# Kernel tuning notes

Measured on AMD Instinct MI355X. Metric: run time of the kernel, lower is better.

The kernel has to match this reference:

```python
import jax, jax.numpy as jnp
import numpy as np

DIM = 1024
NUM_HEADS = 16
HEAD_DIM = DIM // NUM_HEADS
SCALE = HEAD_DIM ** -0.5


def setup_inputs() -> dict:
    key = jax.random.key(0)
    k1, k2, k3, k4 = jax.random.split(key, 4)
    x = jax.random.normal(k1, (4, 2048, DIM), dtype=jnp.float32)
    # nn.Linear weights: out = x @ W.T + b ; store as [out, in] like torch
    w_qkv = jax.random.normal(k2, (3 * DIM, DIM), dtype=jnp.float32) * (DIM ** -0.5)
    w_proj = jax.random.normal(k3, (DIM, DIM), dtype=jnp.float32) * (DIM ** -0.5)
    b_proj = jax.random.normal(k4, (DIM,), dtype=jnp.float32) * 0.01
    return {"x": x, "w_qkv": w_qkv, "w_proj": w_proj, "b_proj": b_proj}


def reference(x, w_qkv, w_proj, b_proj):
    B, N, C = x.shape
    H, D = NUM_HEADS, HEAD_DIM
    qkv = jnp.einsum('bnc,oc->bno', x, w_qkv)            # [B,N,3C]
    qkv = qkv.reshape(B, N, 3, H, D).transpose(2, 0, 3, 1, 4)  # [3,B,H,N,D]
    q, k, v = qkv[0] * SCALE, qkv[1], qkv[2]
    attn = jax.nn.softmax(jnp.einsum('bhnd,bhmd->bhnm', q, k), axis=-1)
    out = jnp.einsum('bhnm,bhmd->bhnd', attn, v)          # [B,H,N,D]
    out = out.transpose(0, 2, 1, 3).reshape(B, N, C)
    return jnp.einsum('bnc,oc->bno', out, w_proj) + b_proj
```

## Files before the change

### kernel.cpp

```cpp
#include <hip/hip_runtime.h>
#include <cstdint>

#define DIM   1024
#define NH    16
#define HD    64
#define SEQ   2048
#define BATCH 4
#define QK_EXP2_SCALE 0.18033688011112042f

typedef _Float16 half8  __attribute__((ext_vector_type(8)));
typedef __fp16   fp16x2 __attribute__((ext_vector_type(2)));
typedef float    f32x4  __attribute__((ext_vector_type(4)));

#define GLOBAL_AS __attribute__((address_space(1)))
#define LDS_AS    __attribute__((address_space(3)))

__device__ __forceinline__ ushort f2h(float f) {
  union { _Float16 h; ushort u; } c; c.h = (_Float16)f; return c.u;
}
__device__ __forceinline__ void async_cp16(const ushort* g, ushort* l) {
  __builtin_amdgcn_global_load_lds((const GLOBAL_AS uint32_t*)g,
                                   (LDS_AS uint32_t*)l, 16, 0, 0);
}

__global__ __launch_bounds__(256) void cvt3_f32_to_f16(
    const float4* __restrict__ x, const float4* __restrict__ wq,
    const float4* __restrict__ wp, ushort4* __restrict__ xo,
    ushort4* __restrict__ wqo, ushort4* __restrict__ wpo) {
  int i = blockIdx.x * 256 + threadIdx.x;
  const float4* src; ushort4* dst; int j;
  if (i < 2097152)      { src = x;  dst = xo;  j = i; }
  else if (i < 2883584) { src = wq; dst = wqo; j = i - 2097152; }
  else                  { src = wp; dst = wpo; j = i - 2883584; }
  float4 v = src[j];
  dst[j] = make_ushort4(f2h(v.x), f2h(v.y), f2h(v.z), f2h(v.w));
}

__global__ __launch_bounds__(256, 2) void gemm_bt256(
    const ushort* __restrict__ A, const ushort* __restrict__ Bt,
    ushort* __restrict__ Ch, int M, int N, int K) {
  __shared__ ushort As[128 * 64];
  __shared__ ushort Bs[256 * 64];
  const int t    = threadIdx.x;
  const int w    = t >> 6;
  const int lane = t & 63;
  const int quad = lane >> 4;
  const int l16  = lane & 15;
  const int wm   = w >> 1, wn = w & 1;

  const int num_n = N >> 8;
  const int SUPER = 8;
  const int bid   = blockIdx.x;
  const int strip = bid / (SUPER * num_n);
  const int rem   = bid % (SUPER * num_n);
  const int m0 = (strip * SUPER + (rem % SUPER)) * 128;
  const int n0 = (rem / SUPER) * 256;

  f32x4 acc[4][8];
  #pragma unroll
  for (int it = 0; it < 4; ++it)
    #pragma unroll
    for (int jt = 0; jt < 8; ++jt) acc[it][jt] = (f32x4){0, 0, 0, 0};

  const int srow = lane >> 3;
  const int scol = ((lane & 7) ^ (lane >> 3)) * 8;
  const int cxa  = l16 & 7;

  for (int k0 = 0; k0 < K; k0 += 64) {
    __syncthreads();
    #pragma unroll
    for (int p = 0; p < 4; ++p) {
      const int rbase = w * 32 + p * 8;
      async_cp16(&A[(size_t)(m0 + rbase + srow) * K + k0 + scol], &As[rbase * 64]);
    }
    #pragma unroll
    for (int p = 0; p < 8; ++p) {
      const int rbase = w * 64 + p * 8;
      async_cp16(&Bt[(size_t)(n0 + rbase + srow) * K + k0 + scol], &Bs[rbase * 64]);
    }
    __syncthreads();
    #pragma unroll
    for (int kk = 0; kk < 2; ++kk) {
      const int ko = ((kk * 4 + quad) ^ cxa) * 8;
      half8 a[4];
      #pragma unroll
      for (int it = 0; it < 4; ++it)
        a[it] = *(const half8*)&As[(wm * 64 + it * 16 + l16) * 64 + ko];
      #pragma unroll
      for (int jt = 0; jt < 8; ++jt) {
        half8 b = *(const half8*)&Bs[(wn * 128 + jt * 16 + l16) * 64 + ko];
        #pragma unroll
        for (int it = 0; it < 4; ++it)
          acc[it][jt] = __builtin_amdgcn_mfma_f32_16x16x32_f16(a[it], b, acc[it][jt], 0, 0, 0);
      }
    }
  }

  #pragma unroll
  for (int it = 0; it < 4; ++it)
    #pragma unroll
    for (int jt = 0; jt < 8; ++jt) {
      const int colbase = n0 + wn * 128 + jt * 16;
      const float qs = (colbase < DIM) ? QK_EXP2_SCALE : 1.0f;
      #pragma unroll
      for (int i = 0; i < 4; ++i) {
        int row = m0 + wm * 64 + it * 16 + quad * 4 + i;
        int col = n0 + wn * 128 + jt * 16 + l16;
        Ch[(size_t)row * N + col] = f2h(acc[it][jt][i] * qs);
      }
    }
}

__global__ __launch_bounds__(256) void gemm_bt128(
    const ushort* __restrict__ A, const ushort* __restrict__ Bt,
    float* __restrict__ Cf, const float* __restrict__ bias,
    int M, int N, int K) {
  __shared__ ushort As[128 * 64];
  __shared__ ushort Bs[128 * 64];
  const int t    = threadIdx.x;
  const int w    = t >> 6;
  const int lane = t & 63;
  const int quad = lane >> 4;
  const int l16  = lane & 15;
  const int wm   = w >> 1, wn = w & 1;

  const int num_n = N >> 7;
  const int SUPER = 8;
  const int bid   = blockIdx.x;
  const int strip = bid / (SUPER * num_n);
  const int rem   = bid % (SUPER * num_n);
  const int m0 = (strip * SUPER + (rem % SUPER)) * 128;
  const int n0 = (rem / SUPER) * 128;

  f32x4 acc[4][4];
  #pragma unroll
  for (int it = 0; it < 4; ++it)
    #pragma unroll
    for (int jt = 0; jt < 4; ++jt) acc[it][jt] = (f32x4){0, 0, 0, 0};

  const int srow = lane >> 3;
  const int scol = ((lane & 7) ^ (lane >> 3)) * 8;
  const int cxa  = l16 & 7;

  for (int k0 = 0; k0 < K; k0 += 64) {
    __syncthreads();
    #pragma unroll
    for (int p = 0; p < 4; ++p) {
      const int rbase = w * 32 + p * 8;
      async_cp16(&A[(size_t)(m0 + rbase + srow) * K + k0 + scol], &As[rbase * 64]);
      async_cp16(&Bt[(size_t)(n0 + rbase + srow) * K + k0 + scol], &Bs[rbase * 64]);
    }
    __syncthreads();
    #pragma unroll
    for (int kk = 0; kk < 2; ++kk) {
      const int ko = ((kk * 4 + quad) ^ cxa) * 8;
      half8 a[4], b[4];
      #pragma unroll
      for (int it = 0; it < 4; ++it)
        a[it] = *(const half8*)&As[(wm * 64 + it * 16 + l16) * 64 + ko];
      #pragma unroll
      for (int jt = 0; jt < 4; ++jt)
        b[jt] = *(const half8*)&Bs[(wn * 64 + jt * 16 + l16) * 64 + ko];
      #pragma unroll
      for (int it = 0; it < 4; ++it)
        #pragma unroll
        for (int jt = 0; jt < 4; ++jt)
          acc[it][jt] = __builtin_amdgcn_mfma_f32_16x16x32_f16(a[it], b[jt], acc[it][jt], 0, 0, 0);
    }
  }

  #pragma unroll
  for (int it = 0; it < 4; ++it)
    #pragma unroll
    for (int jt = 0; jt < 4; ++jt)
      #pragma unroll
      for (int i = 0; i < 4; ++i) {
        int row = m0 + wm * 64 + it * 16 + quad * 4 + i;
        int col = n0 + wn * 64 + jt * 16 + l16;
        Cf[(size_t)row * N + col] = acc[it][jt][i] + bias[col];
      }
}

__global__ __launch_bounds__(256, 2) void attn_mfma(
    const ushort* __restrict__ qkv, ushort* __restrict__ attn_out) {
  constexpr int LDT = 68;
  constexpr int NT  = SEQ / 64;
  __shared__ ushort Qs[256 * LDT];
  __shared__ ushort Ks[2][64 * LDT];
  __shared__ ushort Vt[2][64 * LDT];

  const int t    = threadIdx.x;
  const int w    = t >> 6;
  const int lane = t & 63;
  const int quad = lane >> 4;
  const int l16  = lane & 15;
  const int q0 = blockIdx.x * 256;
  const int h  = blockIdx.y;
  const int b  = blockIdx.z;

  const int srow = t >> 2;
  const int sseg = t & 3;
  const int vp   = t & 31;
  const int vs   = t >> 5;
  const int vpos = ((vp >> 4) << 5) + (((vp >> 1) & 3) << 3)
                 + (((vp >> 3) & 1) << 2) + ((vp & 1) << 1);

  #pragma unroll
  for (int pass = 0; pass < 2; ++pass) {
    const int qrow = pass * 128 + (t >> 1), qseg = t & 1;
    const ushort* qp = qkv + (size_t)(b * SEQ + q0 + qrow) * (3 * DIM)
                       + h * HD + qseg * 32;
    #pragma unroll
    for (int e = 0; e < 4; ++e)
      *(int4*)&Qs[qrow * LDT + qseg * 32 + e * 8] = *(const int4*)(qp + e * 8);
  }

  f32x4 ot[4][4];
  float lacc[4] = {0.0f, 0.0f, 0.0f, 0.0f};
  #pragma unroll
  for (int qt = 0; qt < 4; ++qt)
    #pragma unroll
    for (int nt = 0; nt < 4; ++nt) ot[qt][nt] = (f32x4){0, 0, 0, 0};

  const ushort* kbase = qkv + (size_t)(b * SEQ + srow) * (3 * DIM)
                        + DIM + h * HD + sseg * 16;
  const ushort* vbase = qkv + (size_t)(b * SEQ + 2 * vp) * (3 * DIM)
                        + 2 * DIM + h * HD + vs * 8;
  const size_t tstep = (size_t)64 * (3 * DIM);

  int4 kr0 = *(const int4*)(kbase + 0);
  int4 kr1 = *(const int4*)(kbase + 8);
  int4 vr0 = *(const int4*)(vbase);
  int4 vr1 = *(const int4*)(vbase + 3 * DIM);
  {
    *(int4*)&Ks[0][srow * LDT + sseg * 16 + 0] = kr0;
    *(int4*)&Ks[0][srow * LDT + sseg * 16 + 8] = kr1;
    union { int4 v; ushort u[8]; } r0, r1;
    r0.v = vr0; r1.v = vr1;
    #pragma unroll
    for (int j = 0; j < 8; ++j) {
      uint pk = (uint)r0.u[j] | ((uint)r1.u[j] << 16);
      *(uint*)&Vt[0][(vs * 8 + j) * LDT + vpos] = pk;
    }
  }

  for (int c = 0; c < NT; ++c) {
    const int buf = c & 1;
    __syncthreads();

    const int cn = (c + 1 < NT) ? (c + 1) : 0;
    {
      const ushort* kp = kbase + (size_t)cn * tstep;
      const ushort* vv = vbase + (size_t)cn * tstep;
      kr0 = *(const int4*)(kp + 0);
      kr1 = *(const int4*)(kp + 8);
      vr0 = *(const int4*)(vv);
      vr1 = *(const int4*)(vv + 3 * DIM);
    }
    __builtin_amdgcn_sched_barrier(0);

    f32x4 st[4][4];
    #pragma unroll
    for (int qt = 0; qt < 4; ++qt)
      #pragma unroll
      for (int kt = 0; kt < 4; ++kt) st[qt][kt] = (f32x4){0, 0, 0, 0};
    __builtin_amdgcn_s_setprio(1);
    #pragma unroll
    for (int kk = 0; kk < 2; ++kk) {
      half8 kfr[4], qfr[4];
      #pragma unroll
      for (int kt = 0; kt < 4; ++kt)
        kfr[kt] = *(const half8*)&Ks[buf][(kt * 16 + l16) * LDT + kk * 32 + quad * 8];
      #pragma unroll
      for (int qt = 0; qt < 4; ++qt)
        qfr[qt] = *(const half8*)&Qs[(w * 64 + qt * 16 + l16) * LDT + kk * 32 + quad * 8];
      #pragma unroll
      for (int qt = 0; qt < 4; ++qt)
        #pragma unroll
        for (int kt = 0; kt < 4; ++kt)
          st[qt][kt] = __builtin_amdgcn_mfma_f32_16x16x32_f16(kfr[kt], qfr[qt], st[qt][kt], 0, 0, 0);
    }
    __builtin_amdgcn_s_setprio(0);

    union { half8 h; uint u[4]; } pf[4][2];
    #pragma unroll
    for (int qt = 0; qt < 4; ++qt) {
      float p[4][4];
      #pragma unroll
      for (int kt = 0; kt < 4; ++kt)
        #pragma unroll
        for (int i = 0; i < 4; ++i) {
          p[kt][i] = __builtin_amdgcn_exp2f(st[qt][kt][i]);
          lacc[qt] += p[kt][i];
        }
      #pragma unroll
      for (int kc = 0; kc < 2; ++kc) {
        union { fp16x2 h; uint u; } c01, c23, c45, c67;
        c01.h = __builtin_amdgcn_cvt_pkrtz(p[2 * kc][0], p[2 * kc][1]);
        c23.h = __builtin_amdgcn_cvt_pkrtz(p[2 * kc][2], p[2 * kc][3]);
        c45.h = __builtin_amdgcn_cvt_pkrtz(p[2 * kc + 1][0], p[2 * kc + 1][1]);
        c67.h = __builtin_amdgcn_cvt_pkrtz(p[2 * kc + 1][2], p[2 * kc + 1][3]);
        pf[qt][kc].u[0] = c01.u; pf[qt][kc].u[1] = c23.u;
        pf[qt][kc].u[2] = c45.u; pf[qt][kc].u[3] = c67.u;
      }
    }

    __builtin_amdgcn_s_setprio(1);
    #pragma unroll
    for (int kc = 0; kc < 2; ++kc) {
      half8 vfr[4];
      #pragma unroll
      for (int nt = 0; nt < 4; ++nt)
        vfr[nt] = *(const half8*)&Vt[buf][(nt * 16 + l16) * LDT + kc * 32 + quad * 8];
      #pragma unroll
      for (int qt = 0; qt < 4; ++qt)
        #pragma unroll
        for (int nt = 0; nt < 4; ++nt)
          ot[qt][nt] = __builtin_amdgcn_mfma_f32_16x16x32_f16(vfr[nt], pf[qt][kc].h, ot[qt][nt], 0, 0, 0);
    }
    __builtin_amdgcn_s_setprio(0);

    {
      const int nb = buf ^ 1;
      *(int4*)&Ks[nb][srow * LDT + sseg * 16 + 0] = kr0;
      *(int4*)&Ks[nb][srow * LDT + sseg * 16 + 8] = kr1;
      union { int4 v; ushort u[8]; } r0, r1;
      r0.v = vr0; r1.v = vr1;
      #pragma unroll
      for (int j = 0; j < 8; ++j) {
        uint pk = (uint)r0.u[j] | ((uint)r1.u[j] << 16);
        *(uint*)&Vt[nb][(vs * 8 + j) * LDT + vpos] = pk;
      }
    }
  }

  __syncthreads();
  #pragma unroll
  for (int qt = 0; qt < 4; ++qt) {
    float lsum = lacc[qt];
    lsum += __shfl_xor(lsum, 16);
    lsum += __shfl_xor(lsum, 32);
    float inv = 1.0f / lsum;
    #pragma unroll
    for (int nt = 0; nt < 4; ++nt)
      #pragma unroll
      for (int i = 0; i < 4; ++i)
        Qs[(w * 64 + qt * 16 + l16) * LDT + nt * 16 + quad * 4 + i] =
            f2h(ot[qt][nt][i] * inv);
  }
  __syncthreads();
  #pragma unroll
  for (int pass = 0; pass < 2; ++pass) {
    const int orow = pass * 128 + (t >> 1), oseg = t & 1;
    size_t gbase = (size_t)(b * SEQ + q0 + orow) * DIM + h * HD + oseg * 32;
    #pragma unroll
    for (int e = 0; e < 4; ++e)
      *(int4*)&attn_out[gbase + e * 8] = *(const int4*)&Qs[orow * LDT + oseg * 32 + e * 8];
  }
}

extern "C" void kernel_launch(void* const* d_in, const int* in_sizes, int n_in,
                              void* d_out, int out_size, void* d_ws, size_t ws_size,
                              hipStream_t stream) {
  const float* x      = (const float*)d_in[0];
  const float* w_qkv  = (const float*)d_in[1];
  const float* w_proj = (const float*)d_in[2];
  const float* b_proj = (const float*)d_in[3];

  char* ws = (char*)d_ws;
  ushort* x_h   = (ushort*)(ws + 0);
  ushort* wq_h  = (ushort*)(ws + 16777216);
  ushort* wp_h  = (ushort*)(ws + 23068672);
  ushort* qkv_h = (ushort*)(ws + 25165824);
  ushort* at_h  = (ushort*)(ws + 75497472);

  cvt3_f32_to_f16<<<12288, 256, 0, stream>>>(
      (const float4*)x, (const float4*)w_qkv, (const float4*)w_proj,
      (ushort4*)x_h, (ushort4*)wq_h, (ushort4*)wp_h);

  gemm_bt256<<<64 * 12, 256, 0, stream>>>(x_h, wq_h, qkv_h, 8192, 3072, 1024);
  attn_mfma<<<dim3(8, 16, 4), 256, 0, stream>>>(qkv_h, at_h);
  gemm_bt128<<<64 * 8, 256, 0, stream>>>(at_h, wp_h, (float*)d_out,
                                         b_proj, 8192, 1024, 1024);
}
```

Before: 262.9 us.

## Restructure attention to 8 waves with register-resident Q and split K/V loaders

The attention kernel goes from 4 to 8 waves per block of 256 queries, each wave handling 32 queries. Q fragments stay in registers instead of LDS, and the LDS shrinks to a shared K/V double buffer. Half the threads load and transpose V while the other half load K, and the global loads now sit after the compute phase rather than being prefetched into registers. The block index is flattened so consecutive blocks cover different heads and batches. The aim is higher occupancy and fewer LDS reads, at the risk of exposing global-load latency because the register prefetch is gone.

```diff
diff --git a/kernel.cpp b/kernel.cpp
--- a/kernel.cpp
+++ b/kernel.cpp
@@ -181,46 +181,32 @@
       }
 }
 
-__global__ __launch_bounds__(256, 2) void attn_mfma(
+__global__ __launch_bounds__(512, 4) void attn_mfma(
     const ushort* __restrict__ qkv, ushort* __restrict__ attn_out) {
   constexpr int LDT = 68;
   constexpr int NT  = SEQ / 64;
-  __shared__ ushort Qs[256 * LDT];
-  __shared__ ushort Ks[2][64 * LDT];
-  __shared__ ushort Vt[2][64 * LDT];
+  __shared__ ushort KV[4 * 64 * LDT];
 
   const int t    = threadIdx.x;
   const int w    = t >> 6;
   const int lane = t & 63;
   const int quad = lane >> 4;
   const int l16  = lane & 15;
-  const int q0 = blockIdx.x * 256;
-  const int h  = blockIdx.y;
-  const int b  = blockIdx.z;
-
-  const int srow = t >> 2;
-  const int sseg = t & 3;
+
+  const int id = blockIdx.x;
+  const int hb = id & 63;
+  const int q0 = (id >> 6) * 256;
+  const int h  = hb & 15;
+  const int b  = hb >> 4;
+
+  const bool vrole = (t < 256);
   const int vp   = t & 31;
-  const int vs   = t >> 5;
+  const int vs   = (t >> 5) & 7;
   const int vpos = ((vp >> 4) << 5) + (((vp >> 1) & 3) << 3)
                  + (((vp >> 3) & 1) << 2) + ((vp & 1) << 1);
-
-  #pragma unroll
-  for (int pass = 0; pass < 2; ++pass) {
-    const int qrow = pass * 128 + (t >> 1), qseg = t & 1;
-    const ushort* qp = qkv + (size_t)(b * SEQ + q0 + qrow) * (3 * DIM)
-                       + h * HD + qseg * 32;
-    #pragma unroll
-    for (int e = 0; e < 4; ++e)
-      *(int4*)&Qs[qrow * LDT + qseg * 32 + e * 8] = *(const int4*)(qp + e * 8);
-  }
-
-  f32x4 ot[4][4];
-  float lacc[4] = {0.0f, 0.0f, 0.0f, 0.0f};
-  #pragma unroll
-  for (int qt = 0; qt < 4; ++qt)
-    #pragma unroll
-    for (int nt = 0; nt < 4; ++nt) ot[qt][nt] = (f32x4){0, 0, 0, 0};
+  const int u    = t & 255;
+  const int srow = u >> 2;
+  const int sseg = u & 3;
 
   const ushort* kbase = qkv + (size_t)(b * SEQ + srow) * (3 * DIM)
                         + DIM + h * HD + sseg * 16;
@@ -228,63 +214,69 @@
                         + 2 * DIM + h * HD + vs * 8;
   const size_t tstep = (size_t)64 * (3 * DIM);
 
-  int4 kr0 = *(const int4*)(kbase + 0);
-  int4 kr1 = *(const int4*)(kbase + 8);
-  int4 vr0 = *(const int4*)(vbase);
-  int4 vr1 = *(const int4*)(vbase + 3 * DIM);
+  half8 qreg[2][2];
+  #pragma unroll
+  for (int qt = 0; qt < 2; ++qt)
+    #pragma unroll
+    for (int kk = 0; kk < 2; ++kk)
+      qreg[qt][kk] = *(const half8*)(qkv
+          + (size_t)(b * SEQ + q0 + w * 32 + qt * 16 + l16) * (3 * DIM)
+          + h * HD + kk * 32 + quad * 8);
+
   {
-    *(int4*)&Ks[0][srow * LDT + sseg * 16 + 0] = kr0;
-    *(int4*)&Ks[0][srow * LDT + sseg * 16 + 8] = kr1;
-    union { int4 v; ushort u[8]; } r0, r1;
-    r0.v = vr0; r1.v = vr1;
-    #pragma unroll
-    for (int j = 0; j < 8; ++j) {
-      uint pk = (uint)r0.u[j] | ((uint)r1.u[j] << 16);
-      *(uint*)&Vt[0][(vs * 8 + j) * LDT + vpos] = pk;
-    }
-  }
+    if (vrole) {
+      union { int4 v; ushort u[8]; } r0, r1;
+      r0.v = *(const int4*)(vbase);
+      r1.v = *(const int4*)(vbase + 3 * DIM);
+      ushort* Vd = &KV[2 * 64 * LDT];
+      #pragma unroll
+      for (int j = 0; j < 8; ++j) {
+        uint pk = (uint)r0.u[j] | ((uint)r1.u[j] << 16);
+        *(uint*)&Vd[(vs * 8 + j) * LDT + vpos] = pk;
+      }
+    } else {
+      ushort* Kd = &KV[0];
+      *(int4*)&Kd[srow * LDT + sseg * 16 + 0] = *(const int4*)(kbase + 0);
+      *(int4*)&Kd[srow * LDT + sseg * 16 + 8] = *(const int4*)(kbase + 8);
+    }
+  }
+
+  f32x4 ot[2][4];
+  float lacc[2] = {0.0f, 0.0f};
+  #pragma unroll
+  for (int qt = 0; qt < 2; ++qt)
+    #pragma unroll
+    for (int nt = 0; nt < 4; ++nt) ot[qt][nt] = (f32x4){0, 0, 0, 0};
 
   for (int c = 0; c < NT; ++c) {
     const int buf = c & 1;
-    __syncthreads();
-
-    const int cn = (c + 1 < NT) ? (c + 1) : 0;
-    {
-      const ushort* kp = kbase + (size_t)cn * tstep;
-      const ushort* vv = vbase + (size_t)cn * tstep;
-      kr0 = *(const int4*)(kp + 0);
-      kr1 = *(const int4*)(kp + 8);
-      vr0 = *(const int4*)(vv);
-      vr1 = *(const int4*)(vv + 3 * DIM);
-    }
-    __builtin_amdgcn_sched_barrier(0);
-
-    f32x4 st[4][4];
-    #pragma unroll
-    for (int qt = 0; qt < 4; ++qt)
+    const ushort* Kb = &KV[buf * 64 * LDT];
+    const ushort* Vb = &KV[(2 + buf) * 64 * LDT];
+    __syncthreads();
+
+    f32x4 st[2][4];
+    #pragma unroll
+    for (int qt = 0; qt < 2; ++qt)
       #pragma unroll
       for (int kt = 0; kt < 4; ++kt) st[qt][kt] = (f32x4){0, 0, 0, 0};
     __builtin_amdgcn_s_setprio(1);
     #pragma unroll
     for (int kk = 0; kk < 2; ++kk) {
-      half8 kfr[4], qfr[4];
+      half8 kfr[4];
       #pragma unroll
       for (int kt = 0; kt < 4; ++kt)
-        kfr[kt] = *(const half8*)&Ks[buf][(kt * 16 + l16) * LDT + kk * 32 + quad * 8];
-      #pragma unroll
-      for (int qt = 0; qt < 4; ++qt)
-        qfr[qt] = *(const half8*)&Qs[(w * 64 + qt * 16 + l16) * LDT + kk * 32 + quad * 8];
-      #pragma unroll
-      for (int qt = 0; qt < 4; ++qt)
+        kfr[kt] = *(const half8*)&Kb[(kt * 16 + l16) * LDT + kk * 32 + quad * 8];
+      #pragma unroll
+      for (int qt = 0; qt < 2; ++qt)
         #pragma unroll
         for (int kt = 0; kt < 4; ++kt)
-          st[qt][kt] = __builtin_amdgcn_mfma_f32_16x16x32_f16(kfr[kt], qfr[qt], st[qt][kt], 0, 0, 0);
+          st[qt][kt] = __builtin_amdgcn_mfma_f32_16x16x32_f16(kfr[kt], qreg[qt][kk], st[qt][kt], 0, 0, 0);
     }
     __builtin_amdgcn_s_setprio(0);
 
-    union { half8 h; uint u[4]; } pf[4][2];
-    #pragma unroll
-    for (int qt = 0; qt < 4; ++qt) {
+    union { half8 h; uint u[4]; } pf[2][2];
+    #pragma unroll
+    for (int qt = 0; qt < 2; ++qt) {
       float p[4][4];
       #pragma unroll
       for (int kt = 0; kt < 4; ++kt)
@@ -311,32 +303,40 @@
       half8 vfr[4];
       #pragma unroll
       for (int nt = 0; nt < 4; ++nt)
-        vfr[nt] = *(const half8*)&Vt[buf][(nt * 16 + l16) * LDT + kc * 32 + quad * 8];
-      #pragma unroll
-      for (int qt = 0; qt < 4; ++qt)
+        vfr[nt] = *(const half8*)&Vb[(nt * 16 + l16) * LDT + kc * 32 + quad * 8];
+      #pragma unroll
+      for (int qt = 0; qt < 2; ++qt)
         #pragma unroll
         for (int nt = 0; nt < 4; ++nt)
           ot[qt][nt] = __builtin_amdgcn_mfma_f32_16x16x32_f16(vfr[nt], pf[qt][kc].h, ot[qt][nt], 0, 0, 0);
     }
     __builtin_amdgcn_s_setprio(0);
 
-    {
+    if (c + 1 < NT) {
       const int nb = buf ^ 1;
-      *(int4*)&Ks[nb][srow * LDT + sseg * 16 + 0] = kr0;
-      *(int4*)&Ks[nb][srow * LDT + sseg * 16 + 8] = kr1;
-      union { int4 v; ushort u[8]; } r0, r1;
-      r0.v = vr0; r1.v = vr1;
-      #pragma unroll
-      for (int j = 0; j < 8; ++j) {
-        uint pk = (uint)r0.u[j] | ((uint)r1.u[j] << 16);
-        *(uint*)&Vt[nb][(vs * 8 + j) * LDT + vpos] = pk;
+      if (vrole) {
+        const ushort* vv = vbase + (size_t)(c + 1) * tstep;
+        union { int4 v; ushort u[8]; } r0, r1;
+        r0.v = *(const int4*)(vv);
+        r1.v = *(const int4*)(vv + 3 * DIM);
+        ushort* Vd = &KV[(2 + nb) * 64 * LDT];
+        #pragma unroll
+        for (int j = 0; j < 8; ++j) {
+          uint pk = (uint)r0.u[j] | ((uint)r1.u[j] << 16);
+          *(uint*)&Vd[(vs * 8 + j) * LDT + vpos] = pk;
+        }
+      } else {
+        const ushort* kp = kbase + (size_t)(c + 1) * tstep;
+        ushort* Kd = &KV[nb * 64 * LDT];
+        *(int4*)&Kd[srow * LDT + sseg * 16 + 0] = *(const int4*)(kp + 0);
+        *(int4*)&Kd[srow * LDT + sseg * 16 + 8] = *(const int4*)(kp + 8);
       }
     }
   }
 
   __syncthreads();
   #pragma unroll
-  for (int qt = 0; qt < 4; ++qt) {
+  for (int qt = 0; qt < 2; ++qt) {
     float lsum = lacc[qt];
     lsum += __shfl_xor(lsum, 16);
     lsum += __shfl_xor(lsum, 32);
@@ -345,17 +345,16 @@
     for (int nt = 0; nt < 4; ++nt)
       #pragma unroll
       for (int i = 0; i < 4; ++i)
-        Qs[(w * 64 + qt * 16 + l16) * LDT + nt * 16 + quad * 4 + i] =
+        KV[(w * 32 + qt * 16 + l16) * LDT + nt * 16 + quad * 4 + i] =
             f2h(ot[qt][nt][i] * inv);
   }
   __syncthreads();
-  #pragma unroll
-  for (int pass = 0; pass < 2; ++pass) {
-    const int orow = pass * 128 + (t >> 1), oseg = t & 1;
+  {
+    const int orow = t >> 1, oseg = t & 1;
     size_t gbase = (size_t)(b * SEQ + q0 + orow) * DIM + h * HD + oseg * 32;
     #pragma unroll
     for (int e = 0; e < 4; ++e)
-      *(int4*)&attn_out[gbase + e * 8] = *(const int4*)&Qs[orow * LDT + oseg * 32 + e * 8];
+      *(int4*)&attn_out[gbase + e * 8] = *(const int4*)&KV[orow * LDT + oseg * 32 + e * 8];
   }
 }
 
@@ -379,7 +378,7 @@
       (ushort4*)x_h, (ushort4*)wq_h, (ushort4*)wp_h);
 
   gemm_bt256<<<64 * 12, 256, 0, stream>>>(x_h, wq_h, qkv_h, 8192, 3072, 1024);
-  attn_mfma<<<dim3(8, 16, 4), 256, 0, stream>>>(qkv_h, at_h);
+  attn_mfma<<<512, 512, 0, stream>>>(qkv_h, at_h);
   gemm_bt128<<<64 * 8, 256, 0, stream>>>(at_h, wp_h, (float*)d_out,
                                          b_proj, 8192, 1024, 1024);
 }
```

New measurement: 426.4 us. 1.62x slower.

## Keep Q in registers and stream 128-key tiles in attention

Applied to the files above, without the earlier changes.

The attention kernel now loads the Q fragments straight into registers rather than staging them in LDS, and processes K/V in 128-key chunks, so half as many barriers are needed. The next tile's global loads are no longer prefetched into registers before compute; they are issued after compute and written directly to LDS. Blocks are linearised so consecutive blocks cover different heads and batches of the same query range, and the occupancy hint of 2 blocks is dropped. The aim is to cut LDS traffic and sync overhead, but it raises register pressure and may expose global load latency that was previously hidden.

```diff
diff --git a/kernel.cpp b/kernel.cpp
--- a/kernel.cpp
+++ b/kernel.cpp
@@ -181,22 +181,24 @@
       }
 }
 
-__global__ __launch_bounds__(256, 2) void attn_mfma(
+__global__ __launch_bounds__(256) void attn_mfma(
     const ushort* __restrict__ qkv, ushort* __restrict__ attn_out) {
-  constexpr int LDT = 68;
-  constexpr int NT  = SEQ / 64;
-  __shared__ ushort Qs[256 * LDT];
-  __shared__ ushort Ks[2][64 * LDT];
-  __shared__ ushort Vt[2][64 * LDT];
+  constexpr int LDK = 68;
+  constexpr int LDV = 132;
+  constexpr int NT  = SEQ / 128;
+  __shared__ ushort SH[2 * 128 * LDK + 2 * 64 * LDV];
 
   const int t    = threadIdx.x;
   const int w    = t >> 6;
   const int lane = t & 63;
   const int quad = lane >> 4;
   const int l16  = lane & 15;
-  const int q0 = blockIdx.x * 256;
-  const int h  = blockIdx.y;
-  const int b  = blockIdx.z;
+
+  const int id = blockIdx.x;
+  const int hb = id & 63;
+  const int q0 = (id >> 6) * 256;
+  const int h  = hb & 15;
+  const int b  = hb >> 4;
 
   const int srow = t >> 2;
   const int sseg = t & 3;
@@ -205,131 +207,140 @@
   const int vpos = ((vp >> 4) << 5) + (((vp >> 1) & 3) << 3)
                  + (((vp >> 3) & 1) << 2) + ((vp & 1) << 1);
 
-  #pragma unroll
-  for (int pass = 0; pass < 2; ++pass) {
-    const int qrow = pass * 128 + (t >> 1), qseg = t & 1;
-    const ushort* qp = qkv + (size_t)(b * SEQ + q0 + qrow) * (3 * DIM)
-                       + h * HD + qseg * 32;
-    #pragma unroll
-    for (int e = 0; e < 4; ++e)
-      *(int4*)&Qs[qrow * LDT + qseg * 32 + e * 8] = *(const int4*)(qp + e * 8);
-  }
-
-  f32x4 ot[4][4];
-  float lacc[4] = {0.0f, 0.0f, 0.0f, 0.0f};
-  #pragma unroll
-  for (int qt = 0; qt < 4; ++qt)
-    #pragma unroll
-    for (int nt = 0; nt < 4; ++nt) ot[qt][nt] = (f32x4){0, 0, 0, 0};
-
   const ushort* kbase = qkv + (size_t)(b * SEQ + srow) * (3 * DIM)
                         + DIM + h * HD + sseg * 16;
   const ushort* vbase = qkv + (size_t)(b * SEQ + 2 * vp) * (3 * DIM)
                         + 2 * DIM + h * HD + vs * 8;
-  const size_t tstep = (size_t)64 * (3 * DIM);
-
-  int4 kr0 = *(const int4*)(kbase + 0);
-  int4 kr1 = *(const int4*)(kbase + 8);
-  int4 vr0 = *(const int4*)(vbase);
-  int4 vr1 = *(const int4*)(vbase + 3 * DIM);
+  const size_t rstep = (size_t)64 * (3 * DIM);
+  const size_t tstep = (size_t)128 * (3 * DIM);
+
+  half8 qreg[4][2];
+  #pragma unroll
+  for (int qt = 0; qt < 4; ++qt)
+    #pragma unroll
+    for (int kk = 0; kk < 2; ++kk)
+      qreg[qt][kk] = *(const half8*)(qkv
+          + (size_t)(b * SEQ + q0 + w * 64 + qt * 16 + l16) * (3 * DIM)
+          + h * HD + kk * 32 + quad * 8);
+
   {
-    *(int4*)&Ks[0][srow * LDT + sseg * 16 + 0] = kr0;
-    *(int4*)&Ks[0][srow * LDT + sseg * 16 + 8] = kr1;
-    union { int4 v; ushort u[8]; } r0, r1;
-    r0.v = vr0; r1.v = vr1;
-    #pragma unroll
-    for (int j = 0; j < 8; ++j) {
-      uint pk = (uint)r0.u[j] | ((uint)r1.u[j] << 16);
-      *(uint*)&Vt[0][(vs * 8 + j) * LDT + vpos] = pk;
-    }
-  }
+    ushort* Kd = &SH[0];
+    ushort* Vd = &SH[2 * 128 * LDK];
+    #pragma unroll
+    for (int r = 0; r < 2; ++r) {
+      const ushort* kp = kbase + (size_t)r * rstep;
+      *(int4*)&Kd[(srow + r * 64) * LDK + sseg * 16 + 0] = *(const int4*)(kp + 0);
+      *(int4*)&Kd[(srow + r * 64) * LDK + sseg * 16 + 8] = *(const int4*)(kp + 8);
+      const ushort* vv = vbase + (size_t)r * rstep;
+      union { int4 v; ushort u[8]; } r0, r1;
+      r0.v = *(const int4*)(vv);
+      r1.v = *(const int4*)(vv + 3 * DIM);
+      #pragma unroll
+      for (int j = 0; j < 8; ++j) {
+        uint pk = (uint)r0.u[j] | ((uint)r1.u[j] << 16);
+        *(uint*)&Vd[(vs * 8 + j) * LDV + r * 64 + vpos] = pk;
+      }
+    }
+  }
+
+  f32x4 ot[4][4];
+  float lacc[4] = {0.0f, 0.0f, 0.0f, 0.0f};
+  #pragma unroll
+  for (int qt = 0; qt < 4; ++qt)
+    #pragma unroll
+    for (int nt = 0; nt < 4; ++nt) ot[qt][nt] = (f32x4){0, 0, 0, 0};
 
   for (int c = 0; c < NT; ++c) {
     const int buf = c & 1;
-    __syncthreads();
-
-    const int cn = (c + 1 < NT) ? (c + 1) : 0;
-    {
-      const ushort* kp = kbase + (size_t)cn * tstep;
-      const ushort* vv = vbase + (size_t)cn * tstep;
-      kr0 = *(const int4*)(kp + 0);
-      kr1 = *(const int4*)(kp + 8);
-      vr0 = *(const int4*)(vv);
-      vr1 = *(const int4*)(vv + 3 * DIM);
-    }
-    __builtin_amdgcn_sched_barrier(0);
-
-    f32x4 st[4][4];
-    #pragma unroll
-    for (int qt = 0; qt < 4; ++qt)
-      #pragma unroll
-      for (int kt = 0; kt < 4; ++kt) st[qt][kt] = (f32x4){0, 0, 0, 0};
-    __builtin_amdgcn_s_setprio(1);
-    #pragma unroll
-    for (int kk = 0; kk < 2; ++kk) {
-      half8 kfr[4], qfr[4];
-      #pragma unroll
-      for (int kt = 0; kt < 4; ++kt)
-        kfr[kt] = *(const half8*)&Ks[buf][(kt * 16 + l16) * LDT + kk * 32 + quad * 8];
+    const ushort* Kb = &SH[buf * 128 * LDK];
+    const ushort* Vb = &SH[2 * 128 * LDK + buf * 64 * LDV];
+    __syncthreads();
+
+    #pragma unroll
+    for (int half = 0; half < 2; ++half) {
+      f32x4 st[4][4];
       #pragma unroll
       for (int qt = 0; qt < 4; ++qt)
-        qfr[qt] = *(const half8*)&Qs[(w * 64 + qt * 16 + l16) * LDT + kk * 32 + quad * 8];
-      #pragma unroll
-      for (int qt = 0; qt < 4; ++qt)
+        #pragma unroll
+        for (int kt = 0; kt < 4; ++kt) st[qt][kt] = (f32x4){0, 0, 0, 0};
+      __builtin_amdgcn_s_setprio(1);
+      #pragma unroll
+      for (int kk = 0; kk < 2; ++kk) {
+        half8 kfr[4];
         #pragma unroll
         for (int kt = 0; kt < 4; ++kt)
-          st[qt][kt] = __builtin_amdgcn_mfma_f32_16x16x32_f16(kfr[kt], qfr[qt], st[qt][kt], 0, 0, 0);
-    }
-    __builtin_amdgcn_s_setprio(0);
-
-    union { half8 h; uint u[4]; } pf[4][2];
-    #pragma unroll
-    for (int qt = 0; qt < 4; ++qt) {
-      float p[4][4];
-      #pragma unroll
-      for (int kt = 0; kt < 4; ++kt)
-        #pragma unroll
-        for (int i = 0; i < 4; ++i) {
-          p[kt][i] = __builtin_amdgcn_exp2f(st[qt][kt][i]);
-          lacc[qt] += p[kt][i];
+          kfr[kt] = *(const half8*)&Kb[(half * 64 + kt * 16 + l16) * LDK
+                                       + kk * 32 + quad * 8];
+        #pragma unroll
+        for (int qt = 0; qt < 4; ++qt)
+          #pragma unroll
+          for (int kt = 0; kt < 4; ++kt)
+            st[qt][kt] = __builtin_amdgcn_mfma_f32_16x16x32_f16(
+                kfr[kt], qreg[qt][kk], st[qt][kt], 0, 0, 0);
+      }
+      __builtin_amdgcn_s_setprio(0);
+
+      union { half8 h; uint u[4]; } pf[4][2];
+      #pragma unroll
+      for (int qt = 0; qt < 4; ++qt) {
+        float p[4][4];
+        #pragma unroll
+        for (int kt = 0; kt < 4; ++kt)
+          #pragma unroll
+          for (int i = 0; i < 4; ++i) {
+            p[kt][i] = __builtin_amdgcn_exp2f(st[qt][kt][i]);
+            lacc[qt] += p[kt][i];
+          }
+        #pragma unroll
+        for (int kc = 0; kc < 2; ++kc) {
+          union { fp16x2 h; uint u; } c01, c23, c45, c67;
+          c01.h = __builtin_amdgcn_cvt_pkrtz(p[2 * kc][0], p[2 * kc][1]);
+          c23.h = __builtin_amdgcn_cvt_pkrtz(p[2 * kc][2], p[2 * kc][3]);
+          c45.h = __builtin_amdgcn_cvt_pkrtz(p[2 * kc + 1][0], p[2 * kc + 1][1]);
+          c67.h = __builtin_amdgcn_cvt_pkrtz(p[2 * kc + 1][2], p[2 * kc + 1][3]);
+          pf[qt][kc].u[0] = c01.u; pf[qt][kc].u[1] = c23.u;
+          pf[qt][kc].u[2] = c45.u; pf[qt][kc].u[3] = c67.u;
         }
+      }
+
+      __builtin_amdgcn_s_setprio(1);
       #pragma unroll
       for (int kc = 0; kc < 2; ++kc) {
-        union { fp16x2 h; uint u; } c01, c23, c45, c67;
-        c01.h = __builtin_amdgcn_cvt_pkrtz(p[2 * kc][0], p[2 * kc][1]);
-        c23.h = __builtin_amdgcn_cvt_pkrtz(p[2 * kc][2], p[2 * kc][3]);
-        c45.h = __builtin_amdgcn_cvt_pkrtz(p[2 * kc + 1][0], p[2 * kc + 1][1]);
-        c67.h = __builtin_amdgcn_cvt_pkrtz(p[2 * kc + 1][2], p[2 * kc + 1][3]);
-        pf[qt][kc].u[0] = c01.u; pf[qt][kc].u[1] = c23.u;
-        pf[qt][kc].u[2] = c45.u; pf[qt][kc].u[3] = c67.u;
-      }
-    }
-
-    __builtin_amdgcn_s_setprio(1);
-    #pragma unroll
-    for (int kc = 0; kc < 2; ++kc) {
-      half8 vfr[4];
-      #pragma unroll
-      for (int nt = 0; nt < 4; ++nt)
-        vfr[nt] = *(const half8*)&Vt[buf][(nt * 16 + l16) * LDT + kc * 32 + quad * 8];
-      #pragma unroll
-      for (int qt = 0; qt < 4; ++qt)
+        half8 vfr[4];
         #pragma unroll
         for (int nt = 0; nt < 4; ++nt)
-          ot[qt][nt] = __builtin_amdgcn_mfma_f32_16x16x32_f16(vfr[nt], pf[qt][kc].h, ot[qt][nt], 0, 0, 0);
-    }
-    __builtin_amdgcn_s_setprio(0);
-
-    {
+          vfr[nt] = *(const half8*)&Vb[(nt * 16 + l16) * LDV
+                                       + half * 64 + kc * 32 + quad * 8];
+        #pragma unroll
+        for (int qt = 0; qt < 4; ++qt)
+          #pragma unroll
+          for (int nt = 0; nt < 4; ++nt)
+            ot[qt][nt] = __builtin_amdgcn_mfma_f32_16x16x32_f16(
+                vfr[nt], pf[qt][kc].h, ot[qt][nt], 0, 0, 0);
+      }
+      __builtin_amdgcn_s_setprio(0);
+    }
+
+    if (c + 1 < NT) {
       const int nb = buf ^ 1;
-      *(int4*)&Ks[nb][srow * LDT + sseg * 16 + 0] = kr0;
-      *(int4*)&Ks[nb][srow * LDT + sseg * 16 + 8] = kr1;
-      union { int4 v; ushort u[8]; } r0, r1;
-      r0.v = vr0; r1.v = vr1;
-      #pragma unroll
-      for (int j = 0; j < 8; ++j) {
-        uint pk = (uint)r0.u[j] | ((uint)r1.u[j] << 16);
-        *(uint*)&Vt[nb][(vs * 8 + j) * LDT + vpos] = pk;
+      ushort* Kd = &SH[nb * 128 * LDK];
+      ushort* Vd = &SH[2 * 128 * LDK + nb * 64 * LDV];
+      const ushort* kp0 = kbase + (size_t)(c + 1) * tstep;
+      const ushort* vv0 = vbase + (size_t)(c + 1) * tstep;
+      #pragma unroll
+      for (int r = 0; r < 2; ++r) {
+        const ushort* kp = kp0 + (size_t)r * rstep;
+        *(int4*)&Kd[(srow + r * 64) * LDK + sseg * 16 + 0] = *(const int4*)(kp + 0);
+        *(int4*)&Kd[(srow + r * 64) * LDK + sseg * 16 + 8] = *(const int4*)(kp + 8);
+        const ushort* vv = vv0 + (size_t)r * rstep;
+        union { int4 v; ushort u[8]; } r0, r1;
+        r0.v = *(const int4*)(vv);
+        r1.v = *(const int4*)(vv + 3 * DIM);
+        #pragma unroll
+        for (int j = 0; j < 8; ++j) {
+          uint pk = (uint)r0.u[j] | ((uint)r1.u[j] << 16);
+          *(uint*)&Vd[(vs * 8 + j) * LDV + r * 64 + vpos] = pk;
+        }
       }
     }
   }
@@ -345,7 +356,7 @@
     for (int nt = 0; nt < 4; ++nt)
       #pragma unroll
       for (int i = 0; i < 4; ++i)
-        Qs[(w * 64 + qt * 16 + l16) * LDT + nt * 16 + quad * 4 + i] =
+        SH[(w * 64 + qt * 16 + l16) * LDK + nt * 16 + quad * 4 + i] =
             f2h(ot[qt][nt][i] * inv);
   }
   __syncthreads();
@@ -355,7 +366,7 @@
     size_t gbase = (size_t)(b * SEQ + q0 + orow) * DIM + h * HD + oseg * 32;
     #pragma unroll
     for (int e = 0; e < 4; ++e)
-      *(int4*)&attn_out[gbase + e * 8] = *(const int4*)&Qs[orow * LDT + oseg * 32 + e * 8];
+      *(int4*)&attn_out[gbase + e * 8] = *(const int4*)&SH[orow * LDK + oseg * 32 + e * 8];
   }
 }
 
@@ -379,7 +390,7 @@
       (ushort4*)x_h, (ushort4*)wq_h, (ushort4*)wp_h);
 
   gemm_bt256<<<64 * 12, 256, 0, stream>>>(x_h, wq_h, qkv_h, 8192, 3072, 1024);
-  attn_mfma<<<dim3(8, 16, 4), 256, 0, stream>>>(qkv_h, at_h);
+  attn_mfma<<<512, 256, 0, stream>>>(qkv_h, at_h);
   gemm_bt128<<<64 * 8, 256, 0, stream>>>(at_h, wp_h, (float*)d_out,
                                          b_proj, 8192, 1024, 1024);
 }
```

New measurement: 346.9 us. 32.0% more time.
